# Kernel optimization log

Measured on AMD Instinct MI355X. Metric: run time of the kernel, lower is better.

## Reference

```python
import jax, jax.numpy as jnp
import numpy as np

BATCH, DIM, L, N = 2, 768, 2048, 16


def setup_inputs() -> dict:
    key = jax.random.key(0)
    ks = jax.random.split(key, 8)
    u = jax.random.normal(ks[0], (BATCH, DIM, L), dtype=jnp.float32)
    delta = jax.random.uniform(ks[1], (BATCH, DIM, L), dtype=jnp.float32)
    # A must be negative for a stable SSM (exp(delta*A) <= 1)
    A = -jax.random.uniform(ks[2], (DIM, N), dtype=jnp.float32, minval=0.5, maxval=1.5)
    B = jax.random.normal(ks[3], (BATCH, N, L), dtype=jnp.float32)
    C = jax.random.normal(ks[4], (BATCH, N, L), dtype=jnp.float32)
    D = jax.random.normal(ks[5], (DIM,), dtype=jnp.float32)
    z = jax.random.normal(ks[6], (BATCH, DIM, L), dtype=jnp.float32)
    delta_bias = 0.1 * jax.random.normal(ks[7], (DIM,), dtype=jnp.float32)
    return {"u": u, "delta": delta, "A": A, "B": B, "C": C,
            "D": D, "z": z, "delta_bias": delta_bias}


def _selective_scan(u, delta, A, B, C, D, z, delta_bias):
    # delta_softplus=True path of mamba_ssm selective_scan_fn
    delta = jax.nn.softplus(delta + delta_bias[None, :, None])  # (b, d, l)
    # discretize: deltaA = exp(delta * A), deltaB_u = delta * B * u
    deltaA = jnp.exp(jnp.einsum('bdl,dn->lbdn', delta, A))          # (l, b, d, n)
    deltaBu = jnp.einsum('bdl,bnl,bdl->lbdn', delta, B, u)          # (l, b, d, n)
    C_t = jnp.transpose(C, (2, 0, 1))                               # (l, b, n)

    def step(x, inp):
        a, bu, c = inp
        x = a * x + bu                                              # (b, d, n)
        y = jnp.einsum('bdn,bn->bd', x, c)                          # (b, d)
        return x, y

    x0 = jnp.zeros((BATCH, DIM, N), dtype=u.dtype)
    _, ys = jax.lax.scan(step, x0, (deltaA, deltaBu, C_t))          # ys: (l, b, d)
    y = jnp.transpose(ys, (1, 2, 0))                                # (b, d, l)
    out = y + u * D[None, :, None]
    out = out * jax.nn.silu(z)
    return out


def reference(u, delta, A, B, C, D, z, delta_bias):
    return _selective_scan(u, delta, A, B, C, D, z, delta_bias)
```

## Files before the change

kernel.cpp:

```cpp
#include <hip/hip_runtime.h>


#define LOG2E 1.4426950408889634f
#define LN2   0.6931471805599453f

constexpr int BATCH = 2, DIM = 768, L = 2048, N = 16;
constexpr int NC = 128, LC = 16;
constexpr int DG = DIM / 64;
constexpr int CPB = 4;
constexpr int CG = NC / CPB;
static_assert(NC * LC == L, "chunking must cover L");

__device__ __forceinline__ float fexp2(float x) { return __builtin_amdgcn_exp2f(x); }

__device__ __forceinline__ float softplus(float v) {
  float s = LN2 * __log2f(1.0f + fexp2(v * LOG2E));
  return (v > 20.0f) ? v : s;
}

__device__ __forceinline__ float silu(float v) {
  return v / (1.0f + fexp2(-v * LOG2E));
}

__global__ __launch_bounds__(256) void k_pass1(
    const float* __restrict__ u, const float* __restrict__ delta,
    const float* __restrict__ A, const float* __restrict__ dbias,
    const float* __restrict__ Bg, float* __restrict__ h, float* __restrict__ Ssum) {
  __shared__ float Bs[N][CPB * LC + 4];
  int blk = blockIdx.x;
  int cg = blk % CG;
  int r = blk / CG;
  int dg = r % DG;
  int b = r / DG;
  int t = threadIdx.x;

  {
    int n = t >> 4, jj = t & 15;
    const float* src = Bg + ((long)(b * N + n)) * L + cg * (CPB * LC) + jj * 4;
    float4 v = *(const float4*)src;
    Bs[n][jj * 4 + 0] = v.x; Bs[n][jj * 4 + 1] = v.y;
    Bs[n][jj * 4 + 2] = v.z; Bs[n][jj * 4 + 3] = v.w;
  }

  int wave = t >> 6, lane = t & 63;
  int c = cg * CPB + wave;
  int d = dg * 64 + lane;

  float A2[N];
#pragma unroll
  for (int q = 0; q < 4; q++) {
    float4 av = *(const float4*)(A + d * N + q * 4);
    A2[q * 4 + 0] = av.x * LOG2E; A2[q * 4 + 1] = av.y * LOG2E;
    A2[q * 4 + 2] = av.z * LOG2E; A2[q * 4 + 3] = av.w * LOG2E;
  }
  float bias = dbias[d];

  long base = ((long)(b * DIM + d)) * L + c * LC;
  float dl[LC], uu[LC];
#pragma unroll
  for (int j4 = 0; j4 < 4; j4++) {
    float4 dv = *(const float4*)(delta + base + j4 * 4);
    float4 uv = *(const float4*)(u + base + j4 * 4);
    dl[j4 * 4 + 0] = dv.x; dl[j4 * 4 + 1] = dv.y; dl[j4 * 4 + 2] = dv.z; dl[j4 * 4 + 3] = dv.w;
    uu[j4 * 4 + 0] = uv.x; uu[j4 * 4 + 1] = uv.y; uu[j4 * 4 + 2] = uv.z; uu[j4 * 4 + 3] = uv.w;
  }

  float sp[LC], S = 0.0f;
#pragma unroll
  for (int j = 0; j < LC; j++) { sp[j] = softplus(dl[j] + bias); S += sp[j]; }

  __syncthreads();

  float x[N];
#pragma unroll
  for (int n = 0; n < N; n++) x[n] = 0.0f;
  int col0 = wave * LC;
#pragma unroll
  for (int j = 0; j < LC; j++) {
    float du = sp[j] * uu[j];
#pragma unroll
    for (int n = 0; n < N; n++) {
      float a = fexp2(sp[j] * A2[n]);
      x[n] = a * x[n] + du * Bs[n][col0 + j];
    }
  }

  long hb = ((long)((b * NC + c) * DIM + d)) * N;
#pragma unroll
  for (int q = 0; q < 4; q++) {
    float4 v; v.x = x[q * 4 + 0]; v.y = x[q * 4 + 1]; v.z = x[q * 4 + 2]; v.w = x[q * 4 + 3];
    *(float4*)(h + hb + q * 4) = v;
  }
  Ssum[(b * NC + c) * DIM + d] = S;
}

__global__ __launch_bounds__(256) void k_pass2(
    float* __restrict__ h, const float* __restrict__ Ssum, const float* __restrict__ A) {
  int g = blockIdx.x * 256 + threadIdx.x;
  int n = g & 15;
  int d = (g >> 4) % DIM;
  int b = g / (16 * DIM);
  float A2 = A[d * N + n] * LOG2E;
  float x = 0.0f;
#pragma unroll 4
  for (int c = 0; c < NC; c++) {
    long idx = ((long)((b * NC + c) * DIM + d)) * N + n;
    float hc = h[idx];
    float Sc = Ssum[(b * NC + c) * DIM + d];
    float xi = x;
    x = fexp2(Sc * A2) * x + hc;
    h[idx] = xi;
  }
}

__global__ __launch_bounds__(256) void k_pass3(
    const float* __restrict__ u, const float* __restrict__ delta,
    const float* __restrict__ A, const float* __restrict__ dbias,
    const float* __restrict__ Bg, const float* __restrict__ Cg,
    const float* __restrict__ Dv, const float* __restrict__ z,
    const float* __restrict__ xinit, float* __restrict__ out) {
  __shared__ float Bs[N][CPB * LC + 4];
  __shared__ float Cs[N][CPB * LC + 4];
  int blk = blockIdx.x;
  int cg = blk % CG;
  int r = blk / CG;
  int dg = r % DG;
  int b = r / DG;
  int t = threadIdx.x;

  {
    int n = t >> 4, jj = t & 15;
    long off = ((long)(b * N + n)) * L + cg * (CPB * LC) + jj * 4;
    float4 v = *(const float4*)(Bg + off);
    Bs[n][jj * 4 + 0] = v.x; Bs[n][jj * 4 + 1] = v.y;
    Bs[n][jj * 4 + 2] = v.z; Bs[n][jj * 4 + 3] = v.w;
    float4 w = *(const float4*)(Cg + off);
    Cs[n][jj * 4 + 0] = w.x; Cs[n][jj * 4 + 1] = w.y;
    Cs[n][jj * 4 + 2] = w.z; Cs[n][jj * 4 + 3] = w.w;
  }

  int wave = t >> 6, lane = t & 63;
  int c = cg * CPB + wave;
  int d = dg * 64 + lane;

  float A2[N];
#pragma unroll
  for (int q = 0; q < 4; q++) {
    float4 av = *(const float4*)(A + d * N + q * 4);
    A2[q * 4 + 0] = av.x * LOG2E; A2[q * 4 + 1] = av.y * LOG2E;
    A2[q * 4 + 2] = av.z * LOG2E; A2[q * 4 + 3] = av.w * LOG2E;
  }
  float bias = dbias[d];
  float Dd = Dv[d];

  long hb = ((long)((b * NC + c) * DIM + d)) * N;
  float x[N];
#pragma unroll
  for (int q = 0; q < 4; q++) {
    float4 v = *(const float4*)(xinit + hb + q * 4);
    x[q * 4 + 0] = v.x; x[q * 4 + 1] = v.y; x[q * 4 + 2] = v.z; x[q * 4 + 3] = v.w;
  }

  long base = ((long)(b * DIM + d)) * L + c * LC;
  float dl[LC], uu[LC];
#pragma unroll
  for (int j4 = 0; j4 < 4; j4++) {
    float4 dv = *(const float4*)(delta + base + j4 * 4);
    float4 uv = *(const float4*)(u + base + j4 * 4);
    dl[j4 * 4 + 0] = dv.x; dl[j4 * 4 + 1] = dv.y; dl[j4 * 4 + 2] = dv.z; dl[j4 * 4 + 3] = dv.w;
    uu[j4 * 4 + 0] = uv.x; uu[j4 * 4 + 1] = uv.y; uu[j4 * 4 + 2] = uv.z; uu[j4 * 4 + 3] = uv.w;
  }

  float sp[LC];
#pragma unroll
  for (int j = 0; j < LC; j++) sp[j] = softplus(dl[j] + bias);

  __syncthreads();

  float y[LC];
  int col0 = wave * LC;
#pragma unroll
  for (int j = 0; j < LC; j++) {
    float du = sp[j] * uu[j];
    float acc = 0.0f;
#pragma unroll
    for (int n = 0; n < N; n++) {
      float a = fexp2(sp[j] * A2[n]);
      x[n] = a * x[n] + du * Bs[n][col0 + j];
      acc += x[n] * Cs[n][col0 + j];
    }
    y[j] = acc;
  }

#pragma unroll
  for (int j4 = 0; j4 < 4; j4++) {
    float4 zv = *(const float4*)(z + base + j4 * 4);
    float4 ov;
    ov.x = (y[j4 * 4 + 0] + uu[j4 * 4 + 0] * Dd) * silu(zv.x);
    ov.y = (y[j4 * 4 + 1] + uu[j4 * 4 + 1] * Dd) * silu(zv.y);
    ov.z = (y[j4 * 4 + 2] + uu[j4 * 4 + 2] * Dd) * silu(zv.z);
    ov.w = (y[j4 * 4 + 3] + uu[j4 * 4 + 3] * Dd) * silu(zv.w);
    *(float4*)(out + base + j4 * 4) = ov;
  }
}

__global__ __launch_bounds__(256) void k_simple(
    const float* __restrict__ u, const float* __restrict__ delta,
    const float* __restrict__ A, const float* __restrict__ dbias,
    const float* __restrict__ Bm, const float* __restrict__ Cm,
    const float* __restrict__ Dv, const float* __restrict__ z,
    float* __restrict__ out) {
  int t = blockIdx.x * 256 + threadIdx.x;
  int n = t % N;
  int bd = t / N;
  int d = bd % DIM;
  int b = bd / DIM;
  float A2 = A[d * N + n] * LOG2E;
  float bias = dbias[d];
  float Dd = Dv[d];
  const float* Bp = Bm + ((long)b * N + n) * L;
  const float* Cp = Cm + ((long)b * N + n) * L;
  long base = (long)bd * L;
  float x = 0.0f;
  for (int l = 0; l < L; l++) {
    float dv = delta[base + l];
    float uv = u[base + l];
    float sp = softplus(dv + bias);
    float a = fexp2(sp * A2);
    x = a * x + sp * uv * Bp[l];
    float y = x * Cp[l];
#pragma unroll
    for (int off = 8; off; off >>= 1) y += __shfl_xor(y, off, 16);
    if (n == 0) {
      float zv = z[base + l];
      out[base + l] = (y + uv * Dd) * silu(zv);
    }
  }
}

extern "C" void kernel_launch(void* const* d_in, const int* in_sizes, int n_in,
                              void* d_out, int out_size, void* d_ws, size_t ws_size,
                              hipStream_t stream) {
  const float* u     = (const float*)d_in[0];
  const float* delta = (const float*)d_in[1];
  const float* A     = (const float*)d_in[2];
  const float* Bm    = (const float*)d_in[3];
  const float* Cm    = (const float*)d_in[4];
  const float* Dv    = (const float*)d_in[5];
  const float* z     = (const float*)d_in[6];
  const float* dbias = (const float*)d_in[7];
  float* out = (float*)d_out;

  const size_t hp = (size_t)BATCH * NC * DIM * N;
  const size_t sp = (size_t)BATCH * NC * DIM;
  const size_t need = (hp + sp) * sizeof(float);

  if (ws_size < need) {
    k_simple<<<(BATCH * DIM * N) / 256, 256, 0, stream>>>(u, delta, A, dbias, Bm, Cm, Dv, z, out);
    return;
  }

  float* h = (float*)d_ws;
  float* S = h + hp;

  const int grid13 = BATCH * DG * CG;
  k_pass1<<<grid13, 256, 0, stream>>>(u, delta, A, dbias, Bm, h, S);
  k_pass2<<<(BATCH * DIM * N) / 256, 256, 0, stream>>>(h, S, A);
  k_pass3<<<grid13, 256, 0, stream>>>(u, delta, A, dbias, Bm, Cm, Dv, z, h, out);
}
```

Before: 140.9 us.

## Stage u/delta tiles through LDS for coalesced loads and transpose h layout

Passes 1 and 3 now load 64x64 tiles of delta and u (and, in pass 3, z) with row-contiguous float4 loads into padded shared memory, and each thread reads its time slice from LDS. Before, each lane read its own 16-element strip spaced L floats apart. The per-chunk state h is re-laid out as (b, chunk, n, d), so writes in pass1, the serial combine in pass2 and reads in pass3 are coalesced across d. Pass3 writes y back through LDS so the output store is also coalesced. The cost is more LDS use and an extra barrier, with launch-bound occupancy hints added.

```diff
diff --git a/kernel.cpp b/kernel.cpp
--- a/kernel.cpp
+++ b/kernel.cpp
@@ -9,198 +9,210 @@
 constexpr int DG = DIM / 64;
 constexpr int CPB = 4;
 constexpr int CG = NC / CPB;
+constexpr int NBLK = BATCH * DG * CG;
+constexpr int NCOMB = BATCH * DIM * N;
 static_assert(NC * LC == L, "chunking must cover L");
 
 __device__ __forceinline__ float fexp2(float x) { return __builtin_amdgcn_exp2f(x); }
-
 __device__ __forceinline__ float softplus(float v) {
   float s = LN2 * __log2f(1.0f + fexp2(v * LOG2E));
   return (v > 20.0f) ? v : s;
 }
-
-__device__ __forceinline__ float silu(float v) {
-  return v / (1.0f + fexp2(-v * LOG2E));
-}
-
-__global__ __launch_bounds__(256) void k_pass1(
+__device__ __forceinline__ float silu(float v) { return v / (1.0f + fexp2(-v * LOG2E)); }
+
+__global__ __launch_bounds__(256, 4) void k_pass1(
     const float* __restrict__ u, const float* __restrict__ delta,
     const float* __restrict__ A, const float* __restrict__ dbias,
-    const float* __restrict__ Bg, float* __restrict__ h, float* __restrict__ Ssum) {
-  __shared__ float Bs[N][CPB * LC + 4];
-  int blk = blockIdx.x;
-  int cg = blk % CG;
-  int r = blk / CG;
-  int dg = r % DG;
-  int b = r / DG;
-  int t = threadIdx.x;
+    const float* __restrict__ Bg, float* __restrict__ h, float* __restrict__ S)
+{
+  __shared__ float ds_[64][65];
+  __shared__ float us[64][65];
+  __shared__ float Bs[N][65];
+
+  const int bid = blockIdx.x, t = threadIdx.x;
+  const int cgi = bid & 31;
+  const int dgb = bid >> 5;
+  const int dg = dgb % DG;
+  const int b = dgb / DG;
+  const int d0 = dg * 64, l0 = cgi * 64;
 
   {
-    int n = t >> 4, jj = t & 15;
-    const float* src = Bg + ((long)(b * N + n)) * L + cg * (CPB * LC) + jj * 4;
-    float4 v = *(const float4*)src;
-    Bs[n][jj * 4 + 0] = v.x; Bs[n][jj * 4 + 1] = v.y;
-    Bs[n][jj * 4 + 2] = v.z; Bs[n][jj * 4 + 3] = v.w;
-  }
-
-  int wave = t >> 6, lane = t & 63;
-  int c = cg * CPB + wave;
-  int d = dg * 64 + lane;
+    const int row16 = t >> 4;
+    const int col4 = (t & 15) * 4;
+#pragma unroll
+    for (int rr = 0; rr < 4; rr++) {
+      int row = row16 + rr * 16;
+      long gof = ((long)(b * DIM + d0 + row)) * L + l0 + col4;
+      *(float4*)&ds_[row][col4] = *(const float4*)(delta + gof);
+      *(float4*)&us[row][col4]  = *(const float4*)(u + gof);
+    }
+    long bof = ((long)(b * N + row16)) * L + l0 + col4;
+    *(float4*)&Bs[row16][col4] = *(const float4*)(Bg + bof);
+  }
+
+  const int w = t >> 6, lane = t & 63;
+  const int c = cgi * CPB + w;
+  const int d = d0 + lane;
 
   float A2[N];
 #pragma unroll
   for (int q = 0; q < 4; q++) {
     float4 av = *(const float4*)(A + d * N + q * 4);
-    A2[q * 4 + 0] = av.x * LOG2E; A2[q * 4 + 1] = av.y * LOG2E;
-    A2[q * 4 + 2] = av.z * LOG2E; A2[q * 4 + 3] = av.w * LOG2E;
-  }
-  float bias = dbias[d];
-
-  long base = ((long)(b * DIM + d)) * L + c * LC;
-  float dl[LC], uu[LC];
-#pragma unroll
-  for (int j4 = 0; j4 < 4; j4++) {
-    float4 dv = *(const float4*)(delta + base + j4 * 4);
-    float4 uv = *(const float4*)(u + base + j4 * 4);
-    dl[j4 * 4 + 0] = dv.x; dl[j4 * 4 + 1] = dv.y; dl[j4 * 4 + 2] = dv.z; dl[j4 * 4 + 3] = dv.w;
-    uu[j4 * 4 + 0] = uv.x; uu[j4 * 4 + 1] = uv.y; uu[j4 * 4 + 2] = uv.z; uu[j4 * 4 + 3] = uv.w;
-  }
-
-  float sp[LC], S = 0.0f;
-#pragma unroll
-  for (int j = 0; j < LC; j++) { sp[j] = softplus(dl[j] + bias); S += sp[j]; }
-
-  __syncthreads();
+    A2[q*4+0] = av.x * LOG2E; A2[q*4+1] = av.y * LOG2E;
+    A2[q*4+2] = av.z * LOG2E; A2[q*4+3] = av.w * LOG2E;
+  }
+  const float bias = dbias[d];
+
+  __syncthreads();
+
+  float sp[LC], uu[LC], Ssum = 0.f;
+#pragma unroll
+  for (int j = 0; j < LC; j++) {
+    float dv = ds_[lane][w * LC + j];
+    uu[j] = us[lane][w * LC + j];
+    sp[j] = softplus(dv + bias);
+    Ssum += sp[j];
+  }
 
   float x[N];
 #pragma unroll
-  for (int n = 0; n < N; n++) x[n] = 0.0f;
-  int col0 = wave * LC;
+  for (int n = 0; n < N; n++) x[n] = 0.f;
 #pragma unroll
   for (int j = 0; j < LC; j++) {
     float du = sp[j] * uu[j];
 #pragma unroll
     for (int n = 0; n < N; n++) {
       float a = fexp2(sp[j] * A2[n]);
-      x[n] = a * x[n] + du * Bs[n][col0 + j];
-    }
-  }
-
-  long hb = ((long)((b * NC + c) * DIM + d)) * N;
-#pragma unroll
-  for (int q = 0; q < 4; q++) {
-    float4 v; v.x = x[q * 4 + 0]; v.y = x[q * 4 + 1]; v.z = x[q * 4 + 2]; v.w = x[q * 4 + 3];
-    *(float4*)(h + hb + q * 4) = v;
-  }
-  Ssum[(b * NC + c) * DIM + d] = S;
+      x[n] = a * x[n] + du * Bs[n][w * LC + j];
+    }
+  }
+
+  const long hb = ((long)(b * NC + c)) * N * DIM + d;
+#pragma unroll
+  for (int n = 0; n < N; n++) h[hb + (long)n * DIM] = x[n];
+  S[(b * NC + c) * DIM + d] = Ssum;
 }
 
 __global__ __launch_bounds__(256) void k_pass2(
-    float* __restrict__ h, const float* __restrict__ Ssum, const float* __restrict__ A) {
+    float* __restrict__ h, const float* __restrict__ S, const float* __restrict__ A)
+{
   int g = blockIdx.x * 256 + threadIdx.x;
-  int n = g & 15;
-  int d = (g >> 4) % DIM;
-  int b = g / (16 * DIM);
-  float A2 = A[d * N + n] * LOG2E;
-  float x = 0.0f;
-#pragma unroll 4
-  for (int c = 0; c < NC; c++) {
-    long idx = ((long)((b * NC + c) * DIM + d)) * N + n;
+  int dd = g % DIM;
+  int r = g / DIM;
+  int n = r & 15;
+  int bb = r >> 4;
+  float a2 = A[dd * N + n] * LOG2E;
+  float x = 0.f;
+#pragma unroll 8
+  for (int cc = 0; cc < NC; cc++) {
+    long idx = (((long)(bb * NC + cc)) * N + n) * DIM + dd;
     float hc = h[idx];
-    float Sc = Ssum[(b * NC + c) * DIM + d];
-    float xi = x;
-    x = fexp2(Sc * A2) * x + hc;
-    h[idx] = xi;
-  }
-}
-
-__global__ __launch_bounds__(256) void k_pass3(
+    float Sc = S[(bb * NC + cc) * DIM + dd];
+    h[idx] = x;
+    x = fexp2(Sc * a2) * x + hc;
+  }
+}
+
+__global__ __launch_bounds__(256, 3) void k_pass3(
     const float* __restrict__ u, const float* __restrict__ delta,
     const float* __restrict__ A, const float* __restrict__ dbias,
     const float* __restrict__ Bg, const float* __restrict__ Cg,
     const float* __restrict__ Dv, const float* __restrict__ z,
-    const float* __restrict__ xinit, float* __restrict__ out) {
-  __shared__ float Bs[N][CPB * LC + 4];
-  __shared__ float Cs[N][CPB * LC + 4];
-  int blk = blockIdx.x;
-  int cg = blk % CG;
-  int r = blk / CG;
-  int dg = r % DG;
-  int b = r / DG;
-  int t = threadIdx.x;
+    const float* __restrict__ xinit, float* __restrict__ out)
+{
+  __shared__ float ds_[64][65];
+  __shared__ float us[64][65];
+  __shared__ float Bs[N][65];
+  __shared__ float Cs[N][65];
+
+  const int bid = blockIdx.x, t = threadIdx.x;
+  const int cgi = bid & 31;
+  const int dgb = bid >> 5;
+  const int dg = dgb % DG;
+  const int b = dgb / DG;
+  const int d0 = dg * 64, l0 = cgi * 64;
 
   {
-    int n = t >> 4, jj = t & 15;
-    long off = ((long)(b * N + n)) * L + cg * (CPB * LC) + jj * 4;
-    float4 v = *(const float4*)(Bg + off);
-    Bs[n][jj * 4 + 0] = v.x; Bs[n][jj * 4 + 1] = v.y;
-    Bs[n][jj * 4 + 2] = v.z; Bs[n][jj * 4 + 3] = v.w;
-    float4 w = *(const float4*)(Cg + off);
-    Cs[n][jj * 4 + 0] = w.x; Cs[n][jj * 4 + 1] = w.y;
-    Cs[n][jj * 4 + 2] = w.z; Cs[n][jj * 4 + 3] = w.w;
-  }
-
-  int wave = t >> 6, lane = t & 63;
-  int c = cg * CPB + wave;
-  int d = dg * 64 + lane;
+    const int row16 = t >> 4;
+    const int col4 = (t & 15) * 4;
+#pragma unroll
+    for (int rr = 0; rr < 4; rr++) {
+      int row = row16 + rr * 16;
+      long gof = ((long)(b * DIM + d0 + row)) * L + l0 + col4;
+      *(float4*)&ds_[row][col4] = *(const float4*)(delta + gof);
+      *(float4*)&us[row][col4]  = *(const float4*)(u + gof);
+    }
+    long bof = ((long)(b * N + row16)) * L + l0 + col4;
+    *(float4*)&Bs[row16][col4] = *(const float4*)(Bg + bof);
+    *(float4*)&Cs[row16][col4] = *(const float4*)(Cg + bof);
+  }
+
+  const int w = t >> 6, lane = t & 63;
+  const int c = cgi * CPB + w;
+  const int d = d0 + lane;
 
   float A2[N];
 #pragma unroll
   for (int q = 0; q < 4; q++) {
     float4 av = *(const float4*)(A + d * N + q * 4);
-    A2[q * 4 + 0] = av.x * LOG2E; A2[q * 4 + 1] = av.y * LOG2E;
-    A2[q * 4 + 2] = av.z * LOG2E; A2[q * 4 + 3] = av.w * LOG2E;
-  }
-  float bias = dbias[d];
-  float Dd = Dv[d];
-
-  long hb = ((long)((b * NC + c) * DIM + d)) * N;
+    A2[q*4+0] = av.x * LOG2E; A2[q*4+1] = av.y * LOG2E;
+    A2[q*4+2] = av.z * LOG2E; A2[q*4+3] = av.w * LOG2E;
+  }
+  const float bias = dbias[d];
+
+  const long hb = ((long)(b * NC + c)) * N * DIM + d;
   float x[N];
 #pragma unroll
-  for (int q = 0; q < 4; q++) {
-    float4 v = *(const float4*)(xinit + hb + q * 4);
-    x[q * 4 + 0] = v.x; x[q * 4 + 1] = v.y; x[q * 4 + 2] = v.z; x[q * 4 + 3] = v.w;
-  }
-
-  long base = ((long)(b * DIM + d)) * L + c * LC;
-  float dl[LC], uu[LC];
-#pragma unroll
-  for (int j4 = 0; j4 < 4; j4++) {
-    float4 dv = *(const float4*)(delta + base + j4 * 4);
-    float4 uv = *(const float4*)(u + base + j4 * 4);
-    dl[j4 * 4 + 0] = dv.x; dl[j4 * 4 + 1] = dv.y; dl[j4 * 4 + 2] = dv.z; dl[j4 * 4 + 3] = dv.w;
-    uu[j4 * 4 + 0] = uv.x; uu[j4 * 4 + 1] = uv.y; uu[j4 * 4 + 2] = uv.z; uu[j4 * 4 + 3] = uv.w;
-  }
-
-  float sp[LC];
-#pragma unroll
-  for (int j = 0; j < LC; j++) sp[j] = softplus(dl[j] + bias);
+  for (int n = 0; n < N; n++) x[n] = xinit[hb + (long)n * DIM];
+
+  __syncthreads();
+
+  float sp[LC], uu[LC];
+#pragma unroll
+  for (int j = 0; j < LC; j++) {
+    float dv = ds_[lane][w * LC + j];
+    uu[j] = us[lane][w * LC + j];
+    sp[j] = softplus(dv + bias);
+  }
 
   __syncthreads();
 
   float y[LC];
-  int col0 = wave * LC;
 #pragma unroll
   for (int j = 0; j < LC; j++) {
     float du = sp[j] * uu[j];
-    float acc = 0.0f;
+    float acc = 0.f;
 #pragma unroll
     for (int n = 0; n < N; n++) {
       float a = fexp2(sp[j] * A2[n]);
-      x[n] = a * x[n] + du * Bs[n][col0 + j];
-      acc += x[n] * Cs[n][col0 + j];
+      x[n] = a * x[n] + du * Bs[n][w * LC + j];
+      acc += x[n] * Cs[n][w * LC + j];
     }
     y[j] = acc;
   }
-
-#pragma unroll
-  for (int j4 = 0; j4 < 4; j4++) {
-    float4 zv = *(const float4*)(z + base + j4 * 4);
-    float4 ov;
-    ov.x = (y[j4 * 4 + 0] + uu[j4 * 4 + 0] * Dd) * silu(zv.x);
-    ov.y = (y[j4 * 4 + 1] + uu[j4 * 4 + 1] * Dd) * silu(zv.y);
-    ov.z = (y[j4 * 4 + 2] + uu[j4 * 4 + 2] * Dd) * silu(zv.z);
-    ov.w = (y[j4 * 4 + 3] + uu[j4 * 4 + 3] * Dd) * silu(zv.w);
-    *(float4*)(out + base + j4 * 4) = ov;
+#pragma unroll
+  for (int j = 0; j < LC; j++) ds_[lane][w * LC + j] = y[j];
+
+  __syncthreads();
+
+  {
+    const int row16 = t >> 4;
+    const int col4 = (t & 15) * 4;
+#pragma unroll
+    for (int rr = 0; rr < 4; rr++) {
+      int row = row16 + rr * 16;
+      long gof = ((long)(b * DIM + d0 + row)) * L + l0 + col4;
+      float4 zv = *(const float4*)(z + gof);
+      float4 yv = *(const float4*)&ds_[row][col4];
+      float4 uv = *(const float4*)&us[row][col4];
+      float Dd = Dv[d0 + row];
+      float4 ov;
+      ov.x = (yv.x + uv.x * Dd) * silu(zv.x);
+      ov.y = (yv.y + uv.y * Dd) * silu(zv.y);
+      ov.z = (yv.z + uv.z * Dd) * silu(zv.z);
+      ov.w = (yv.w + uv.w * Dd) * silu(zv.w);
+      *(float4*)(out + gof) = ov;
+    }
   }
 }
 
@@ -252,8 +264,8 @@
   float* out = (float*)d_out;
 
   const size_t hp = (size_t)BATCH * NC * DIM * N;
-  const size_t sp = (size_t)BATCH * NC * DIM;
-  const size_t need = (hp + sp) * sizeof(float);
+  const size_t spn = (size_t)BATCH * NC * DIM;
+  const size_t need = (hp + spn) * sizeof(float);
 
   if (ws_size < need) {
     k_simple<<<(BATCH * DIM * N) / 256, 256, 0, stream>>>(u, delta, A, dbias, Bm, Cm, Dv, z, out);
@@ -263,8 +275,7 @@
   float* h = (float*)d_ws;
   float* S = h + hp;
 
-  const int grid13 = BATCH * DG * CG;
-  k_pass1<<<grid13, 256, 0, stream>>>(u, delta, A, dbias, Bm, h, S);
-  k_pass2<<<(BATCH * DIM * N) / 256, 256, 0, stream>>>(h, S, A);
-  k_pass3<<<grid13, 256, 0, stream>>>(u, delta, A, dbias, Bm, Cm, Dv, z, h, out);
-}
+  k_pass1<<<NBLK, 256, 0, stream>>>(u, delta, A, dbias, Bm, h, S);
+  k_pass2<<<NCOMB / 256, 256, 0, stream>>>(h, S, A);
+  k_pass3<<<NBLK, 256, 0, stream>>>(u, delta, A, dbias, Bm, Cm, Dv, z, h, out);
+}
```

Result: faster. 130.7 us (-7.2%).
